# Kernel tuning notes

Measured on AMD Instinct MI355X. Metric: run time of the kernel, lower is better.

The kernel has to match this reference:

```python
import jax, jax.numpy as jnp
import numpy as np

H = W = 1024          # image_shape (square)
ZP, PH, PW = 16, 32, 32   # psf z-stack shape
THRESH = 2.0          # detection_threshold
K = 1024              # spots_per_frame
ROISIZE = PW          # default roisize = psf.shape[-1]
BG_R = PW * 2         # default bg_filter_size
MAXF = PW             # default max_filter_size


def setup_inputs() -> dict:
    key = jax.random.key(0)
    k1, k2 = jax.random.split(key)
    image = jax.random.uniform(k1, (H, W), jnp.float32) * 100.0
    psf = jax.random.uniform(k2, (ZP, PH, PW), jnp.float32)
    psf = psf / jnp.sum(psf, axis=(1, 2), keepdims=True)  # normalized PSF stack
    return {"image": image, "psf": psf}


def _precompute_filters(psf):
    pad = (H - PH) // 2  # square image/psf -> same pad both dims
    psf_padded = jnp.pad(psf, ((0, 0), (pad, pad), (pad, pad)))
    psf_padded = jnp.fft.fftshift(psf_padded, axes=(1, 2))
    psf_fd = jnp.flip(jnp.fft.fft2(psf_padded), axis=(1, 2))
    rr = (jnp.arange(H) - H // 2)[:, None] ** 2 + (jnp.arange(W) - W // 2)[None, :] ** 2
    bg = (rr < BG_R ** 2).astype(jnp.float32) / (np.pi * BG_R ** 2)
    bg_fd = jnp.fft.fft2(jnp.fft.fftshift(bg))
    return psf_fd, bg_fd


def reference(image, psf):
    psf_fd, bg_fd = _precompute_filters(psf)
    image_fd = jnp.fft.fft2(image)
    conv_psf = jnp.fft.ifft2(image_fd[None] * psf_fd).real       # [Z,H,W]
    conv_bg = jnp.fft.ifft2(image_fd * bg_fd).real               # [H,W]
    ratio = conv_psf / (conv_bg[None] + 1.0)                     # matched-filter SNR
    result = ratio.max(axis=0)                                   # [H,W]
    zmap = jnp.argmax(ratio, axis=0)                             # best z plane

    # MaxPool2d(MAXF, stride=1, padding=MAXF//2-1): torch pads with -inf,
    # output is [H-1,W-1]; torch code then zero-pads one row/col at top-left.
    p = MAXF // 2 - 1
    mx = jax.lax.reduce_window(result, -jnp.inf, jax.lax.max,
                               (MAXF, MAXF), (1, 1), ((p, p), (p, p)))
    mx = jnp.pad(mx, ((1, 0), (1, 0)))                           # back to [H,W]

    mask = jnp.where((mx == result) & (result > THRESH), result, 0.0)
    values, indices = jax.lax.top_k(mask.ravel(), K)
    x = indices % W
    y = indices // H  # torch divides by input_shape[0]; square so == W
    roy = y - ROISIZE // 2
    rox = x - ROISIZE // 2
    valid = ((values > THRESH)
             & (roy >= 0) & (roy < H - ROISIZE)
             & (rox >= 0) & (rox < W - ROISIZE))

    # fixed-shape version of boolean select: clamp for safe gather, mask invalids
    roy_c = jnp.clip(roy, 0, H - ROISIZE)
    rox_c = jnp.clip(rox, 0, W - ROISIZE)
    r = jnp.arange(ROISIZE)
    Y = roy_c[:, None, None] + r[None, :, None]                  # [K,R,1]
    X = rox_c[:, None, None] + r[None, None, :]                  # [K,1,R]
    rois = image[Y, X] * valid[:, None, None].astype(image.dtype)  # [K,R,R]

    roipos = jnp.stack((roy_c, rox_c), -1) * valid[:, None]
    intensity = values * valid
    return roipos, intensity, rois, valid
```

## Files before the change

### kernel.cpp

```cpp
#include <hip/hip_runtime.h>
#include <stdint.h>

typedef float v4f __attribute__((ext_vector_type(4)));
typedef float f2u __attribute__((ext_vector_type(2), aligned(4)));

#define PEX_STRIDE 1156
#define CSTRIDE 858
#define WS_IMG8   0
#define WS_BFRAG  1048576
#define WS_PEX    1064960
#define WS_RB     5799936
#define WS_RESULT 9994240
#define WS_CAND   14188544

__device__ inline unsigned char f32_to_e4m3(float v) {
    if (!(v > 0.0f)) return 0;
    if (v >= 448.0f) return 0x7e;
    if (v < 0.015625f) {
        int m = (int)(v * 512.0f + 0.5f);
        if (m > 7) return 0x08;
        return (unsigned char)m;
    }
    unsigned int u = __float_as_uint(v) + 0x00080000u;
    int e = (int)((u >> 23) & 0xff) - 127;
    int m3 = (int)(u >> 20) & 7;
    int e8 = e + 7;
    if (e8 >= 16) return 0x7e;
    return (unsigned char)((e8 << 3) | m3);
}

__global__ void k_pex(const float* __restrict__ img, float* __restrict__ pex,
                      uint32_t* __restrict__ img8, const float* __restrict__ psf,
                      unsigned char* __restrict__ bf, unsigned int* cnt,
                      float4* __restrict__ out, int n4) {
    __shared__ float wtot[4];
    int blk = blockIdx.x, t = threadIdx.x;
    if (blk >= 1024) {
        if (blk < 2080) {
            int i = (blk - 1024) * 256 + t;
            if (i < n4) { float4 z; z.x = z.y = z.z = z.w = 0.f; out[i] = z; }
        } else {
            int u = (blk - 2080) * 256 + t;
            if (u == 0) cnt[0] = 0u;
            int kb = u >> 9; int l = (u >> 3) & 63; int j = u & 7;
            int z = l & 15; int q = l >> 4;
            int a = kb; int b = q * 8 + j;
            float p = psf[z * 1024 + a * 32 + b];
            float c = cosf((float)(a + b - 32) * (6.283185307179586f / 1024.0f));
            bf[kb * 512 + l * 8 + j] = f32_to_e4m3(p * c * 1024.0f);
        }
        return;
    }
    int r = blk;
    const float* row = img + r * 1024;
    float s[5];
    float acc = 0.f;
    int base = t * 5;
    #pragma unroll
    for (int j = 0; j < 5; j++) {
        int c = base + j;
        float v = (c < 1152) ? row[(c - 64) & 1023] : 0.f;
        acc += v; s[j] = acc;
    }
    float sc = acc;
    int lane = t & 63, w = t >> 6;
    #pragma unroll
    for (int off = 1; off < 64; off <<= 1) {
        float v = __shfl_up(sc, off, 64);
        if (lane >= off) sc += v;
    }
    if (lane == 63) wtot[w] = sc;
    __syncthreads();
    float wbase = 0.f;
    #pragma unroll
    for (int i = 0; i < 3; i++) if (i < w) wbase += wtot[i];
    float excl = wbase + (sc - acc);
    float* prow = pex + r * PEX_STRIDE;
    if (t == 0) prow[0] = 0.f;
    #pragma unroll
    for (int j = 0; j < 5; j++) {
        int c = base + j;
        if (c < 1152) prow[c + 1] = excl + s[j];
    }
    float4 v4 = *(const float4*)(row + 4 * t);
    img8[r * 256 + t] = (uint32_t)f32_to_e4m3(v4.x)
                      | ((uint32_t)f32_to_e4m3(v4.y) << 8)
                      | ((uint32_t)f32_to_e4m3(v4.z) << 16)
                      | ((uint32_t)f32_to_e4m3(v4.w) << 24);
}

__global__ __launch_bounds__(256) void k_bg(const float* __restrict__ pex,
                                            float* __restrict__ rb) {
    static constexpr int W[64] = {
        63,63,63,63,63,63,63,63,63,63,63,63,
        62,62,62,62, 61,61,61,61, 60,60,60, 59,59, 58,58,58, 57,57, 56,
        55,55, 54,54, 53, 52,52, 51, 50, 49,49,
        48,47,46,45,44,43,42,41,
        39,38,37,35,34,32,30,29,27,24,22,19,15,11
    };
    int blk = blockIdx.x;
    int xcd = blk & 7;
    int sub = blk >> 4;
    int half = (blk >> 3) & 1;
    int s = xcd * 16 + sub;
    int row = s * 8 + 3;
    int n0 = (half << 9) + ((int)threadIdx.x << 1);
    f2u acc0, acc1;
    {
        const float* pr = pex + row * PEX_STRIDE + n0;
        acc0 = *(const f2u*)(pr + 128) - *(const f2u*)(pr + 1);
        acc1 = (f2u)0.f;
    }
    #pragma unroll 3
    for (int dy = 1; dy <= 63; dy++) {
        const int w = W[dy];
        const float* p1 = pex + ((row - dy) & 1023) * PEX_STRIDE + n0;
        const float* p2 = pex + ((row + dy) & 1023) * PEX_STRIDE + n0;
        acc0 += *(const f2u*)(p1 + 65 + w) - *(const f2u*)(p1 + 64 - w);
        acc1 += *(const f2u*)(p2 + 65 + w) - *(const f2u*)(p2 + 64 - w);
    }
    f2u sum = acc0 + acc1;
    const float k = (float)(1.0 / (3.14159265358979323846 * 4096.0));
    f2u r2;
    r2.x = 1.0f / ((sum.x * k + 1.0f) * 1024.0f);
    r2.y = 1.0f / ((sum.y * k + 1.0f) * 1024.0f);
    *(f2u*)(rb + s * 1024 + n0) = r2;
}

__global__ __launch_bounds__(512, 2) void k_conv(
    const unsigned long long* __restrict__ img64,
    const unsigned long long* __restrict__ bfrag,
    const float* __restrict__ rb, float* __restrict__ result) {
    __shared__ unsigned long long sm[8 * CSTRIDE];
    int tid = threadIdx.x;
    int wave = tid >> 6, lane = tid & 63;
    int b = blockIdx.x;
    int tr = b >> 5, tc = b & 31;
    int r0 = tr * 64, c0 = tc * 32;

    for (int u = tid; u < 665; u += 512) {
        int dr = u / 7;
        int x8 = u - dr * 7;
        int row = (r0 + dr - 16) & 1023;
        int cb0 = (c0 + x8 * 8 - 16) & 1023;
        int cb1 = (cb0 + 8) & 1023;
        unsigned long long lo = img64[row * 128 + (cb0 >> 3)];
        unsigned long long hi = img64[row * 128 + (cb1 >> 3)];
        int dst = dr * 9 + x8;
        sm[dst] = lo;
        #pragma unroll
        for (int s = 1; s < 8; s++)
            sm[s * CSTRIDE + dst] = (lo >> (8 * s)) | (hi << (64 - 8 * s));
    }
    __syncthreads();

    int i0 = (wave >> 1) * 16;
    int cw = (wave & 1) * 16;
    int g = lane >> 4;
    int slot = ((cw + (lane & 15)) >> 3) + g;
    const unsigned long long* bp = sm + (lane & 7) * CSTRIDE + slot + i0 * 9;

    v4f acc[16];
    #pragma unroll
    for (int f = 0; f < 16; f++) acc[f] = (v4f)0.0f;

    unsigned long long anext = bfrag[lane];
    for (int kb = 0; kb < 32; kb++) {
        unsigned long long acur = anext;
        anext = bfrag[((kb < 31 ? kb + 1 : 31) << 6) + lane];
        const unsigned long long* pk = bp + kb * 9;
        #pragma unroll
        for (int cc = 0; cc < 16; cc += 2) {
            unsigned long long b0 = pk[cc * 9];
            unsigned long long b1 = pk[cc * 9 + 9];
            acc[cc]     = __builtin_amdgcn_mfma_f32_16x16x32_fp8_fp8(
                (long)acur, (long)b0, acc[cc], 0, 0, 0);
            acc[cc + 1] = __builtin_amdgcn_mfma_f32_16x16x32_fp8_fp8(
                (long)acur, (long)b1, acc[cc + 1], 0, 0, 0);
        }
    }

    float zmax[16];
    #pragma unroll
    for (int cc = 0; cc < 16; cc++) {
        v4f v = acc[cc];
        float m = fmaxf(fmaxf(v.x, v.y), fmaxf(v.z, v.w));
        m = fmaxf(m, __shfl_xor(m, 16, 64));
        m = fmaxf(m, __shfl_xor(m, 32, 64));
        zmax[cc] = m;
    }
    int gcol = c0 + cw + (lane & 15);
    #pragma unroll
    for (int c4 = 0; c4 < 4; c4++) {
        float m01 = (g & 1) ? zmax[c4 * 4 + 1] : zmax[c4 * 4 + 0];
        float m23 = (g & 1) ? zmax[c4 * 4 + 3] : zmax[c4 * 4 + 2];
        float m = (g & 2) ? m23 : m01;
        int grow = r0 + i0 + c4 * 4 + g;
        result[grow * 1024 + gcol] = m * rb[(grow >> 3) * 1024 + gcol];
    }
}

__global__ __launch_bounds__(256) void k_maxcand(const float* __restrict__ result,
                                                 unsigned int* cnt,
                                                 unsigned long long* cand) {
    __shared__ float ls[95 * 96];
    __shared__ float hr[95 * 64];
    __shared__ float wmax[4];
    int bx = blockIdx.x & 15, by = blockIdx.x >> 4;
    int i0 = by * 64, j0 = bx * 64;
    int t = threadIdx.x;
    const float4* cb4 = (const float4*)(result + i0 * 1024 + j0);
    float mx = -3.4e38f;
    #pragma unroll
    for (int k = 0; k < 4; k++) {
        int idx = k * 256 + t;
        float4 v = cb4[(idx >> 4) * 256 + (idx & 15)];
        mx = fmaxf(mx, fmaxf(fmaxf(v.x, v.y), fmaxf(v.z, v.w)));
    }
    #pragma unroll
    for (int m = 1; m < 64; m <<= 1) mx = fmaxf(mx, __shfl_xor(mx, m, 64));
    if ((t & 63) == 0) wmax[t >> 6] = mx;
    __syncthreads();
    float tmax = fmaxf(fmaxf(wmax[0], wmax[1]), fmaxf(wmax[2], wmax[3]));
    if (tmax <= 2.0f) return;

    for (int idx = t; idx < 95 * 95; idx += 256) {
        int r = idx / 95, c = idx - r * 95;
        int gr = i0 - 16 + r, gc = j0 - 16 + c;
        float v = -3.4e38f;
        if ((unsigned)gr < 1024u && (unsigned)gc < 1024u) v = result[gr * 1024 + gc];
        ls[r * 96 + c] = v;
    }
    __syncthreads();
    for (int idx = t; idx < 95 * 64; idx += 256) {
        int r = idx >> 6, c = idx & 63;
        const float* p = ls + r * 96 + c;
        float m = p[0];
        #pragma unroll
        for (int d = 1; d < 32; d++) m = fmaxf(m, p[d]);
        hr[idx] = m;
    }
    __syncthreads();
    for (int idx = t; idx < 64 * 64; idx += 256) {
        int r = idx >> 6, c = idx & 63;
        const float* p = hr + r * 64 + c;
        float m = p[0];
        #pragma unroll
        for (int d = 1; d < 32; d++) m = fmaxf(m, p[d * 64]);
        float v = ls[(r + 16) * 96 + (c + 16)];
        int gi = i0 + r, gj = j0 + c;
        if (gi >= 1 && gj >= 1 && v > 2.0f && v == m) {
            unsigned int k = atomicAdd(cnt, 1u);
            if (k < 2048)
                cand[k] = ((unsigned long long)__float_as_uint(v) << 32)
                        | (unsigned int)(~(unsigned int)(gi * 1024 + gj));
        }
    }
}

__global__ __launch_bounds__(1024) void k_final(
    const float* __restrict__ image, const unsigned int* __restrict__ cnt,
    const unsigned long long* __restrict__ cand, float* __restrict__ out) {
    __shared__ unsigned long long keys[2048];
    int t = threadIdx.x;
    int n = (int)cnt[0]; if (n > 2048) n = 2048;
    if (n == 0) return;
    for (int k = t; k < 2048; k += 1024) keys[k] = (k < n) ? cand[k] : 0ull;
    __syncthreads();
    for (int size = 2; size <= 2048; size <<= 1) {
        for (int stride = size >> 1; stride > 0; stride >>= 1) {
            for (int i = t; i < 2048; i += 1024) {
                int ixj = i ^ stride;
                if (ixj > i) {
                    unsigned long long a = keys[i], b = keys[ixj];
                    bool sw = ((i & size) == 0) ? (a < b) : (a > b);
                    if (sw) { keys[i] = b; keys[ixj] = a; }
                }
            }
            __syncthreads();
        }
    }
    float* roipos = out;
    float* intensity = out + 2048;
    float* rois = out + 3072;
    float* validf = out + 3072 + 1048576;
    int nw = n < 1024 ? n : 1024;
    if (t < nw) {
        unsigned long long key = keys[t];
        float val = __uint_as_float((unsigned int)(key >> 32));
        unsigned int p = ~(unsigned int)key;
        int y = (int)(p >> 10), x = (int)(p & 1023);
        int roy = y - 16, rox = x - 16;
        bool valid = (roy >= 0 && roy < 992 && rox >= 0 && rox < 992);
        int royc = roy < 0 ? 0 : (roy > 992 ? 992 : roy);
        int roxc = rox < 0 ? 0 : (rox > 992 ? 992 : rox);
        roipos[2 * t]     = valid ? (float)royc : 0.f;
        roipos[2 * t + 1] = valid ? (float)roxc : 0.f;
        intensity[t]      = valid ? val : 0.f;
        validf[t]         = valid ? 1.f : 0.f;
    }
    __syncthreads();
    for (int k = 0; k < nw; k++) {
        unsigned long long key = keys[k];
        unsigned int p = ~(unsigned int)key;
        int y = (int)(p >> 10), x = (int)(p & 1023);
        int roy = y - 16, rox = x - 16;
        if (!(roy >= 0 && roy < 992 && rox >= 0 && rox < 992)) continue;
        int u = t >> 5, vv = t & 31;
        rois[k * 1024 + t] = image[(roy + u) * 1024 + (rox + vv)];
    }
}

extern "C" void kernel_launch(void* const* d_in, const int* in_sizes, int n_in,
                              void* d_out, int out_size, void* d_ws, size_t ws_size,
                              hipStream_t stream) {
    const float* image = (const float*)d_in[0];
    const float* psf   = (const float*)d_in[1];
    float* out = (float*)d_out;
    char* ws = (char*)d_ws;
    unsigned char* img8  = (unsigned char*)(ws + WS_IMG8);
    unsigned char* bfrag = (unsigned char*)(ws + WS_BFRAG);
    float* pex = (float*)(ws + WS_PEX);
    float* rb  = (float*)(ws + WS_RB);
    float* result = (float*)(ws + WS_RESULT);
    unsigned int* cnt = (unsigned int*)(ws + WS_CAND);
    unsigned long long* cand = (unsigned long long*)(ws + WS_CAND + 16);

    int n4 = out_size / 4;
    hipLaunchKernelGGL(k_pex,     dim3(2144), dim3(256), 0, stream,
                       image, pex, (uint32_t*)img8, psf, bfrag, cnt, (float4*)d_out, n4);
    hipLaunchKernelGGL(k_bg,      dim3(256),  dim3(256), 0, stream, pex, rb);
    hipLaunchKernelGGL(k_conv,    dim3(512),  dim3(512), 0, stream,
                       (const unsigned long long*)img8, (const unsigned long long*)bfrag, rb, result);
    hipLaunchKernelGGL(k_maxcand, dim3(256),  dim3(256), 0, stream, result, cnt, cand);
    hipLaunchKernelGGL(k_final,   dim3(1),    dim3(1024), 0, stream, image, cnt, cand, out);
}
```

Baseline: 102.1 us.

## Reuse B fragments via register sliding window in conv; widen bg grid

k_conv keeps a 16-entry register window of B fragments and rotates through it. Each k-step then loads only one new LDS value instead of sixteen, since consecutive k-blocks share rows offset by one. Launch bounds are raised to 4 blocks per CU, which tightens the register budget for the larger live set. k_bg switches from two floats per thread to one and doubles the grid to 512 blocks for more parallelism.

```diff
diff --git a/kernel.cpp b/kernel.cpp
--- a/kernel.cpp
+++ b/kernel.cpp
@@ -2,7 +2,6 @@
 #include <stdint.h>
 
 typedef float v4f __attribute__((ext_vector_type(4)));
-typedef float f2u __attribute__((ext_vector_type(2), aligned(4)));
 
 #define PEX_STRIDE 1156
 #define CSTRIDE 858
@@ -100,34 +99,31 @@
     };
     int blk = blockIdx.x;
     int xcd = blk & 7;
-    int sub = blk >> 4;
-    int half = (blk >> 3) & 1;
+    int quarter = (blk >> 3) & 3;
+    int sub = blk >> 5;
     int s = xcd * 16 + sub;
     int row = s * 8 + 3;
-    int n0 = (half << 9) + ((int)threadIdx.x << 1);
-    f2u acc0, acc1;
+    int n0 = (quarter << 8) + (int)threadIdx.x;
+    float acc0, acc1;
     {
         const float* pr = pex + row * PEX_STRIDE + n0;
-        acc0 = *(const f2u*)(pr + 128) - *(const f2u*)(pr + 1);
-        acc1 = (f2u)0.f;
+        acc0 = pr[128] - pr[1];
+        acc1 = 0.f;
     }
     #pragma unroll 3
     for (int dy = 1; dy <= 63; dy++) {
         const int w = W[dy];
         const float* p1 = pex + ((row - dy) & 1023) * PEX_STRIDE + n0;
         const float* p2 = pex + ((row + dy) & 1023) * PEX_STRIDE + n0;
-        acc0 += *(const f2u*)(p1 + 65 + w) - *(const f2u*)(p1 + 64 - w);
-        acc1 += *(const f2u*)(p2 + 65 + w) - *(const f2u*)(p2 + 64 - w);
-    }
-    f2u sum = acc0 + acc1;
+        acc0 += p1[65 + w] - p1[64 - w];
+        acc1 += p2[65 + w] - p2[64 - w];
+    }
+    float sum = acc0 + acc1;
     const float k = (float)(1.0 / (3.14159265358979323846 * 4096.0));
-    f2u r2;
-    r2.x = 1.0f / ((sum.x * k + 1.0f) * 1024.0f);
-    r2.y = 1.0f / ((sum.y * k + 1.0f) * 1024.0f);
-    *(f2u*)(rb + s * 1024 + n0) = r2;
-}
-
-__global__ __launch_bounds__(512, 2) void k_conv(
+    rb[s * 1024 + n0] = 1.0f / ((sum * k + 1.0f) * 1024.0f);
+}
+
+__global__ __launch_bounds__(512, 4) void k_conv(
     const unsigned long long* __restrict__ img64,
     const unsigned long long* __restrict__ bfrag,
     const float* __restrict__ rb, float* __restrict__ result) {
@@ -164,19 +160,24 @@
     #pragma unroll
     for (int f = 0; f < 16; f++) acc[f] = (v4f)0.0f;
 
+    unsigned long long bwin[16];
+    #pragma unroll
+    for (int s = 0; s < 16; s++) bwin[s] = bp[s * 9];
+
     unsigned long long anext = bfrag[lane];
-    for (int kb = 0; kb < 32; kb++) {
-        unsigned long long acur = anext;
-        anext = bfrag[((kb < 31 ? kb + 1 : 31) << 6) + lane];
-        const unsigned long long* pk = bp + kb * 9;
+    for (int kbo = 0; kbo < 32; kbo += 16) {
         #pragma unroll
-        for (int cc = 0; cc < 16; cc += 2) {
-            unsigned long long b0 = pk[cc * 9];
-            unsigned long long b1 = pk[cc * 9 + 9];
-            acc[cc]     = __builtin_amdgcn_mfma_f32_16x16x32_fp8_fp8(
-                (long)acur, (long)b0, acc[cc], 0, 0, 0);
-            acc[cc + 1] = __builtin_amdgcn_mfma_f32_16x16x32_fp8_fp8(
-                (long)acur, (long)b1, acc[cc + 1], 0, 0, 0);
+        for (int kk = 0; kk < 16; kk++) {
+            int kb = kbo + kk;
+            unsigned long long acur = anext;
+            anext = bfrag[((kb < 31 ? kb + 1 : 31) << 6) + lane];
+            unsigned long long nb = bp[(kb < 31 ? kb + 16 : 46) * 9];
+            #pragma unroll
+            for (int cc = 0; cc < 16; cc++) {
+                acc[cc] = __builtin_amdgcn_mfma_f32_16x16x32_fp8_fp8(
+                    (long)acur, (long)bwin[(kk + cc) & 15], acc[cc], 0, 0, 0);
+            }
+            bwin[kk & 15] = nb;
         }
     }
 
@@ -329,7 +330,7 @@
     int n4 = out_size / 4;
     hipLaunchKernelGGL(k_pex,     dim3(2144), dim3(256), 0, stream,
                        image, pex, (uint32_t*)img8, psf, bfrag, cnt, (float4*)d_out, n4);
-    hipLaunchKernelGGL(k_bg,      dim3(256),  dim3(256), 0, stream, pex, rb);
+    hipLaunchKernelGGL(k_bg,      dim3(512),  dim3(256), 0, stream, pex, rb);
     hipLaunchKernelGGL(k_conv,    dim3(512),  dim3(512), 0, stream,
                        (const unsigned long long*)img8, (const unsigned long long*)bfrag, rb, result);
     hipLaunchKernelGGL(k_maxcand, dim3(256),  dim3(256), 0, stream, result, cnt, cand);
```

Measured after the change: 100.1 us. Within noise of the previous version (-1.9%).
